# Kernel tuning notes

Hardware: AMD Instinct MI355X
Metric: run time of the kernel (lower is better)

## Reference

```python
import jax, jax.numpy as jnp
import numpy as np

D_STATE = 16
D_CONV = 4


def layernorm(x, g, b, eps=1e-5):
    mu = jnp.mean(x, axis=-1, keepdims=True)
    var = jnp.mean(jnp.square(x - mu), axis=-1, keepdims=True)
    return (x - mu) * jax.lax.rsqrt(var + eps) * g + b


def mamba(x, W_in, conv_w, conv_b, W_x, W_dt, b_dt, A_log, D_param, W_out):
    # x: (B, L, C)
    B, L, C = x.shape
    d_inner, d_conv = conv_w.shape
    d_state = A_log.shape[1]
    dt_rank = W_dt.shape[0]

    xz = x @ W_in                       # (B, L, 2*d_inner)
    xm, z = jnp.split(xz, 2, axis=-1)   # each (B, L, d_inner)

    # depthwise causal conv1d (padding d_conv-1 on the left, truncated to L)
    xp = jnp.pad(xm, ((0, 0), (d_conv - 1, 0), (0, 0)))
    xm = sum(xp[:, k:k + L, :] * conv_w[:, k] for k in range(d_conv)) + conv_b
    xm = jax.nn.silu(xm)

    dbl = xm @ W_x                      # (B, L, dt_rank + 2*d_state)
    dt, Bm, Cm = jnp.split(dbl, [dt_rank, dt_rank + d_state], axis=-1)
    dt = jax.nn.softplus(dt @ W_dt + b_dt)  # (B, L, d_inner)
    A = -jnp.exp(A_log)                     # (d_inner, d_state)

    def step(h, inputs):
        dt_t, B_t, C_t, x_t = inputs        # (B,d_inner),(B,d_state),(B,d_state),(B,d_inner)
        dA = jnp.exp(dt_t[..., None] * A)   # (B, d_inner, d_state)
        h = dA * h + (dt_t * x_t)[..., None] * B_t[:, None, :]
        y = jnp.einsum('bds,bs->bd', h, C_t)
        return h, y

    seq = (dt.transpose(1, 0, 2), Bm.transpose(1, 0, 2),
           Cm.transpose(1, 0, 2), xm.transpose(1, 0, 2))
    h0 = jnp.zeros((B, d_inner, d_state), x.dtype)
    _, ys = jax.lax.scan(step, h0, seq)     # ys: (L, B, d_inner)
    y = ys.transpose(1, 0, 2) + xm * D_param
    y = y * jax.nn.silu(z)
    return y @ W_out                        # (B, L, C)


def setup_inputs() -> dict:
    key = jax.random.key(0)
    B, C, H, W = 8, 256, 32, 32
    d_inner = 2 * C
    dt_rank = (C + 15) // 16  # 16
    hidden = 4 * C
    ks = jax.random.split(key, 12)
    s = lambda k, shape, scale=0.02: jax.random.normal(k, shape, jnp.float32) * scale
    return {
        'x': jax.random.normal(ks[0], (B, C, H, W), jnp.float32),
        'ln1_g': jnp.ones((C,), jnp.float32), 'ln1_b': jnp.zeros((C,), jnp.float32),
        'ln2_g': jnp.ones((C,), jnp.float32), 'ln2_b': jnp.zeros((C,), jnp.float32),
        'W_in': s(ks[1], (C, 2 * d_inner)),
        'conv_w': s(ks[2], (d_inner, D_CONV), 0.1),
        'conv_b': jnp.zeros((d_inner,), jnp.float32),
        'W_x': s(ks[3], (d_inner, dt_rank + 2 * D_STATE)),
        'W_dt': s(ks[4], (dt_rank, d_inner)),
        'b_dt': s(ks[5], (d_inner,), 0.1),
        'A_log': jnp.log(jnp.tile(jnp.arange(1, D_STATE + 1, dtype=jnp.float32), (d_inner, 1))),
        'D_param': jnp.ones((d_inner,), jnp.float32),
        'W_out': s(ks[6], (d_inner, C)),
        'W1': s(ks[7], (C, hidden)), 'b1': jnp.zeros((hidden,), jnp.float32),
        'W2': s(ks[8], (hidden, C)), 'b2': jnp.zeros((C,), jnp.float32),
    }


def reference(x, ln1_g, ln1_b, ln2_g, ln2_b, W_in, conv_w, conv_b, W_x, W_dt,
              b_dt, A_log, D_param, W_out, W1, b1, W2, b2):
    B, C, H, W = x.shape
    x = x.transpose(0, 2, 3, 1)          # (B, H, W, C)
    res = x
    xn = layernorm(x, ln1_g, ln1_b)
    xm = mamba(xn.reshape(B, H * W, C), W_in, conv_w, conv_b, W_x, W_dt,
               b_dt, A_log, D_param, W_out).reshape(B, H, W, C)
    x = xm + res
    res = x
    xn = layernorm(x, ln2_g, ln2_b)
    x = jax.nn.gelu(xn @ W1 + b1, approximate=False) @ W2 + b2 + res
    return x.transpose(0, 3, 1, 2)        # (B, C, H, W)
```

## Files before the change

### kernel.cpp

```cpp
#include <hip/hip_runtime.h>
#include <hip/hip_bf16.h>
#include <math.h>

using u16 = unsigned short;
using u32 = unsigned int;
typedef __attribute__((ext_vector_type(8))) short bf16x8;
typedef __attribute__((ext_vector_type(4))) float f32x4;
typedef __attribute__((ext_vector_type(8))) unsigned short us8;
typedef __attribute__((ext_vector_type(4))) unsigned short us4;

__device__ __forceinline__ float b2f(u16 u) {
  return __uint_as_float(((u32)u) << 16);
}
__device__ __forceinline__ u16 f2b(float f) {
  u32 x = __float_as_uint(f);
  x += 0x7fffu + ((x >> 16) & 1u);
  return (u16)(x >> 16);
}

__global__ void k_detect(const u16* __restrict__ alog, int* __restrict__ flag) {
  if (threadIdx.x == 0 && blockIdx.x == 0)
    flag[0] = (alog[1] != 0) ? 1 : 0;
}

__device__ __forceinline__ u16 cvt_one(const void* src, int i, int f) {
  u16 r;
  if (f == 0) {
    float v = ((const float*)src)[i];
    if (!isfinite(v)) v = 0.f;
    r = f2b(v);
  } else {
    r = ((const u16*)src)[i];
    if (((r >> 7) & 0xFFu) == 0xFFu) r = 0;
  }
  return r;
}

__global__ __launch_bounds__(256) void k_cvtw(const void* __restrict__ s0,
    const void* __restrict__ s1, const void* __restrict__ s2,
    const void* __restrict__ s3, u16* __restrict__ d0, u16* __restrict__ d1,
    u16* __restrict__ d2, u16* __restrict__ d3, const int* __restrict__ flag) {
  int i = blockIdx.x * 256 + threadIdx.x;
  int f = flag[0];
  if (i < 262144) {
    int k = i >> 10, n = i & 1023;
    d0[n * 256 + k] = cvt_one(s0, i, f);
  } else if (i < 524288) {
    int j = i - 262144; int k = j >> 10, n = j & 1023;
    d1[n * 256 + k] = cvt_one(s1, j, f);
  } else if (i < 786432) {
    int j = i - 524288; int k = j >> 8, n = j & 255;
    d2[n * 1024 + k] = cvt_one(s2, j, f);
  } else if (i < 917504) {
    int j = i - 786432; int k = j >> 8, n = j & 255;
    d3[n * 512 + k] = cvt_one(s3, j, f);
  }
}

struct SmallCvt {
  const void* src[13];
  u16* dst[13];
  int end[13];
};
__global__ __launch_bounds__(256) void k_cvt_small(SmallCvt p,
    int total, const int* __restrict__ flag) {
  int i = blockIdx.x * 256 + threadIdx.x;
  if (i >= total) return;
  int f = flag[0];
  int seg = 0, base = 0;
  #pragma unroll
  for (int s = 0; s < 13; ++s) {
    if (i >= p.end[s]) { seg = s + 1; base = p.end[s]; }
  }
  p.dst[seg][i - base] = cvt_one(p.src[seg], i - base, f);
}

__global__ __launch_bounds__(256) void k_tln(const void* __restrict__ src,
    const u16* __restrict__ g, const u16* __restrict__ be,
    u16* __restrict__ xt, u16* __restrict__ xn, const int* __restrict__ flag) {
  __shared__ float t[256][33];
  __shared__ float smu[32], srs[32];
  int bid = blockIdx.x;
  int lt = bid & 31, b = bid >> 5;
  int f = flag[0];
  int lc = threadIdx.x & 31, lr = threadIdx.x >> 5;
  for (int i = 0; i < 32; ++i) {
    int c = i * 8 + lr;
    int l = lt * 32 + lc;
    size_t idx = ((size_t)b * 256 + c) * 1024 + l;
    float v;
    if (f == 0) {
      v = ((const float*)src)[idx];
      if (!isfinite(v)) v = 0.f;
    } else {
      u16 u = ((const u16*)src)[idx];
      if (((u >> 7) & 0xFFu) == 0xFFu) u = 0;
      v = b2f(u);
    }
    t[c][lc] = v;
  }
  __syncthreads();
  int tok = threadIdx.x >> 3, j = threadIdx.x & 7;
  float s = 0.f, q = 0.f;
  for (int k = 0; k < 32; ++k) {
    float v = t[j + 8 * k][tok];
    s += v; q = fmaf(v, v, q);
  }
  s += __shfl_xor(s, 1, 8); q += __shfl_xor(q, 1, 8);
  s += __shfl_xor(s, 2, 8); q += __shfl_xor(q, 2, 8);
  s += __shfl_xor(s, 4, 8); q += __shfl_xor(q, 4, 8);
  if (j == 0) {
    float mu = s * (1.f / 256.f);
    smu[tok] = mu;
    srs[tok] = rsqrtf(q * (1.f / 256.f) - mu * mu + 1e-5f);
  }
  __syncthreads();
  float gv = b2f(g[threadIdx.x]), bv = b2f(be[threadIdx.x]);
  size_t tok0 = (size_t)b * 1024 + lt * 32;
  for (int i = 0; i < 32; ++i) {
    float v = t[threadIdx.x][i];
    size_t o = (tok0 + i) * 256 + threadIdx.x;
    xt[o] = f2b(v);
    xn[o] = f2b((v - smu[i]) * srs[i] * gv + bv);
  }
}

__global__ __launch_bounds__(256) void k_tout(const u16* __restrict__ ytmp,
    void* __restrict__ outp, const int* __restrict__ flag) {
  __shared__ float t[32][33];
  int bid = blockIdx.x;
  int lt = bid & 31, ct = (bid >> 5) & 7, b = bid >> 8;
  int f = flag[0];
  int lc = threadIdx.x & 31, lr = threadIdx.x >> 5;
  #pragma unroll
  for (int r = 0; r < 4; ++r) {
    int l = lt * 32 + lr + r * 8;
    int c = ct * 32 + lc;
    t[lr + r * 8][lc] = b2f(ytmp[((size_t)b * 1024 + l) * 256 + c]);
  }
  __syncthreads();
  #pragma unroll
  for (int r = 0; r < 4; ++r) {
    int c = ct * 32 + lr + r * 8;
    int l = lt * 32 + lc;
    size_t oi = ((size_t)b * 256 + c) * 1024 + l;
    float v = t[lc][lr + r * 8];
    if (f) ((u16*)outp)[oi] = f2b(v);
    else   ((float*)outp)[oi] = v;
  }
}

__global__ __launch_bounds__(256) void k_ln(const u16* __restrict__ xin,
    const u16* __restrict__ g, const u16* __restrict__ be,
    u16* __restrict__ xn) {
  __shared__ float buf[256];
  __shared__ float mv[2];
  int tok = blockIdx.x;
  int c = threadIdx.x;
  float v = b2f(xin[(size_t)tok * 256 + c]);
  buf[c] = v;
  __syncthreads();
  for (int off = 128; off > 0; off >>= 1) {
    if (c < off) buf[c] += buf[c + off];
    __syncthreads();
  }
  if (c == 0) mv[0] = buf[0] * (1.f / 256.f);
  __syncthreads();
  float mu = mv[0];
  float dd = v - mu;
  buf[c] = dd * dd;
  __syncthreads();
  for (int off = 128; off > 0; off >>= 1) {
    if (c < off) buf[c] += buf[c + off];
    __syncthreads();
  }
  if (c == 0) mv[1] = rsqrtf(buf[0] * (1.f / 256.f) + 1e-5f);
  __syncthreads();
  float rs = mv[1];
  xn[(size_t)tok * 256 + c] = f2b(dd * rs * b2f(g[c]) + b2f(be[c]));
}

__global__ __launch_bounds__(256) void k_conv(const u16* __restrict__ xz,
    const u16* __restrict__ cw, const u16* __restrict__ cb,
    u16* __restrict__ xm) {
  int idx = blockIdx.x * 256 + threadIdx.x;
  int d4 = (idx & 127) * 4;
  int tok = idx >> 7;
  int l = tok & 1023;
  float a[4];
  #pragma unroll
  for (int j = 0; j < 4; ++j) a[j] = b2f(cb[d4 + j]);
  #pragma unroll
  for (int k = 0; k < 4; ++k) {
    int ls = l - 3 + k;
    if (ls >= 0) {
      us4 xv = *(const us4*)&xz[(size_t)(tok - 3 + k) * 1024 + d4];
      #pragma unroll
      for (int j = 0; j < 4; ++j)
        a[j] = fmaf(b2f(xv[j]), b2f(cw[(d4 + j) * 4 + k]), a[j]);
    }
  }
  us4 o;
  #pragma unroll
  for (int j = 0; j < 4; ++j) {
    float sig = 1.f / (1.f + __expf(-a[j]));
    o[j] = f2b(a[j] * sig);
  }
  *(us4*)&xm[(size_t)tok * 512 + d4] = o;
}

__global__ __launch_bounds__(256) void k_wc(const u16* __restrict__ Wx,
    const u16* __restrict__ Wdt, u16* __restrict__ wcbc) {
  int idx = blockIdx.x * 256 + threadIdx.x;
  int j = idx >> 9, i = idx & 511;
  u16 r;
  if (j < 512) {
    float s = 0.f;
    #pragma unroll
    for (int k = 0; k < 16; ++k)
      s = fmaf(b2f(Wx[i * 48 + k]), b2f(Wdt[k * 512 + j]), s);
    r = f2b(s);
  } else if (j < 544) {
    r = Wx[i * 48 + 16 + (j - 512)];
  } else {
    r = 0;
  }
  wcbc[idx] = r;
}

__global__ __launch_bounds__(256) void k_scan1(const u16* __restrict__ dt,
    const u16* __restrict__ xm, const u16* __restrict__ bc,
    const u16* __restrict__ A_log, u16* __restrict__ hend,
    float* __restrict__ sdtw) {
  __shared__ float sB[32][16];
  int bi = blockIdx.x;
  int half = bi & 1;
  int bc_ = bi >> 1;
  int b = bc_ >> 5, c = bc_ & 31;
  int d = half * 256 + threadIdx.x;
  size_t tok0 = (size_t)b * 1024 + c * 32;
  for (int i = threadIdx.x; i < 512; i += 256) {
    int t = i >> 4, s = i & 15;
    sB[t][s] = b2f(bc[(tok0 + t) * 32 + s]);
  }
  __syncthreads();
  float As[16], h[16];
  bool fast = true;
  #pragma unroll
  for (int s = 0; s < 16; ++s) {
    As[s] = -__expf(b2f(A_log[d * 16 + s]));
    h[s] = 0.f;
    fast = fast && (fabsf(As[s] + (float)(s + 1)) < 0.02f * (s + 1));
  }
  float sacc = 0.f;
  float dtv = b2f(dt[tok0 * 512 + d]);
  float xv  = b2f(xm[tok0 * 512 + d]);
  if (fast) {
    for (int t = 0; t < 32; ++t) {
      float ndt = 0.f, nx = 0.f;
      if (t < 31) {
        ndt = b2f(dt[(tok0 + t + 1) * 512 + d]);
        nx  = b2f(xm[(tok0 + t + 1) * 512 + d]);
      }
      sacc += dtv;
      float u = dtv * xv;
      float q = __expf(-dtv), p = 1.f;
      #pragma unroll
      for (int s = 0; s < 16; ++s) {
        p *= q;
        h[s] = fmaf(p, h[s], u * sB[t][s]);
      }
      dtv = ndt; xv = nx;
    }
  } else {
    for (int t = 0; t < 32; ++t) {
      float ndt = 0.f, nx = 0.f;
      if (t < 31) {
        ndt = b2f(dt[(tok0 + t + 1) * 512 + d]);
        nx  = b2f(xm[(tok0 + t + 1) * 512 + d]);
      }
      sacc += dtv;
      float u = dtv * xv;
      #pragma unroll
      for (int s = 0; s < 16; ++s)
        h[s] = fmaf(__expf(dtv * As[s]), h[s], u * sB[t][s]);
      dtv = ndt; xv = nx;
    }
  }
  u16* hp = hend + ((size_t)bc_ * 512 + d) * 16;
  #pragma unroll
  for (int s = 0; s < 16; ++s) hp[s] = f2b(h[s]);
  sdtw[(size_t)bc_ * 512 + d] = sacc;
}

__global__ __launch_bounds__(256) void k_scan2(u16* __restrict__ hend,
    const float* __restrict__ sdtw, const u16* __restrict__ A_log) {
  int idx = blockIdx.x * 256 + threadIdx.x;
  int s = idx & 15, d = (idx >> 4) & 511, b = idx >> 13;
  float As_ = -__expf(b2f(A_log[d * 16 + s]));
  if (fabsf(As_ + (float)(s + 1)) < 0.02f * (s + 1)) As_ = -(float)(s + 1);
  float H = 0.f;
  for (int c = 0; c < 32; ++c) {
    size_t off = (size_t)(b * 32 + c) * 512 + d;
    float dec = __expf(As_ * sdtw[off]);
    float he = b2f(hend[off * 16 + s]);
    hend[off * 16 + s] = f2b(H);
    H = fmaf(dec, H, he);
  }
}

__global__ __launch_bounds__(256) void k_scan3(const u16* __restrict__ dt,
    const u16* __restrict__ xm, const u16* __restrict__ bc,
    const u16* __restrict__ xz, const u16* __restrict__ A_log,
    const u16* __restrict__ Dp, const u16* __restrict__ hstart,
    u16* __restrict__ yg) {
  __shared__ float sB[32][16], sC[32][16];
  int bi = blockIdx.x;
  int half = bi & 1;
  int bc_ = bi >> 1;
  int b = bc_ >> 5, c = bc_ & 31;
  int d = half * 256 + threadIdx.x;
  size_t tok0 = (size_t)b * 1024 + c * 32;
  for (int i = threadIdx.x; i < 1024; i += 256) {
    int t = i >> 5, col = i & 31;
    float v = b2f(bc[(tok0 + t) * 32 + col]);
    if (col < 16) sB[t][col] = v;
    else          sC[t][col - 16] = v;
  }
  __syncthreads();
  float As[16], h[16];
  const u16* hp = hstart + ((size_t)bc_ * 512 + d) * 16;
  bool fast = true;
  #pragma unroll
  for (int s = 0; s < 16; ++s) {
    As[s] = -__expf(b2f(A_log[d * 16 + s]));
    h[s] = b2f(hp[s]);
    fast = fast && (fabsf(As[s] + (float)(s + 1)) < 0.02f * (s + 1));
  }
  float Dd = b2f(Dp[d]);
  float dtv = b2f(dt[tok0 * 512 + d]);
  float xv  = b2f(xm[tok0 * 512 + d]);
  float zv  = b2f(xz[tok0 * 1024 + 512 + d]);
  for (int t = 0; t < 32; ++t) {
    float ndt = 0.f, nx = 0.f, nz = 0.f;
    if (t < 31) {
      ndt = b2f(dt[(tok0 + t + 1) * 512 + d]);
      nx  = b2f(xm[(tok0 + t + 1) * 512 + d]);
      nz  = b2f(xz[(tok0 + t + 1) * 1024 + 512 + d]);
    }
    float u = dtv * xv;
    if (fast) {
      float q = __expf(-dtv), p = 1.f;
      #pragma unroll
      for (int s = 0; s < 16; ++s) {
        p *= q;
        h[s] = fmaf(p, h[s], u * sB[t][s]);
      }
    } else {
      #pragma unroll
      for (int s = 0; s < 16; ++s)
        h[s] = fmaf(__expf(dtv * As[s]), h[s], u * sB[t][s]);
    }
    float y0 = 0.f, y1 = 0.f, y2 = 0.f, y3 = 0.f;
    #pragma unroll
    for (int s = 0; s < 16; s += 4) {
      y0 = fmaf(h[s + 0], sC[t][s + 0], y0);
      y1 = fmaf(h[s + 1], sC[t][s + 1], y1);
      y2 = fmaf(h[s + 2], sC[t][s + 2], y2);
      y3 = fmaf(h[s + 3], sC[t][s + 3], y3);
    }
    float y = (y0 + y1) + (y2 + y3);
    float yy = fmaf(xv, Dd, y);
    float sig = 1.f / (1.f + __expf(-zv));
    yg[(tok0 + t) * 512 + d] = f2b(yy * zv * sig);
    dtv = ndt; xv = nx; zv = nz;
  }
}

template<int EPI, int BM, int BN>
__global__ __launch_bounds__(256) void k_mgemm(
    const u16* __restrict__ A, const u16* __restrict__ Bt,
    const u16* __restrict__ bias, const u16* __restrict__ res,
    u16* __restrict__ outp, u16* __restrict__ out2, int M, int N, int K) {
  constexpr int BK = 32;
  constexpr int LDP = BK + 8;
  constexpr int MT = BM / 32, NT = BN / 32;
  constexpr int AL = (BM * BK) / 2048, BL = (BN * BK) / 2048;
  __shared__ u16 As[BM][LDP];
  __shared__ u16 Bs[BN][LDP];
  const int tid = threadIdx.x;
  const int wid = tid >> 6, lane = tid & 63;
  const int wr = wid >> 1, wc2 = wid & 1;
  const int lrow = lane & 15, lk = lane >> 4;
  const int m0 = blockIdx.y * BM, n0 = blockIdx.x * BN;

  f32x4 acc[MT][NT];
  #pragma unroll
  for (int i = 0; i < MT; ++i)
    #pragma unroll
    for (int j = 0; j < NT; ++j)
      acc[i][j] = (f32x4){0.f, 0.f, 0.f, 0.f};

  us8 ra[AL], rb[BL];
  #pragma unroll
  for (int i = 0; i < AL; ++i) {
    int c = tid + i * 256, row = c >> 2, k0 = (c & 3) * 8;
    ra[i] = *(const us8*)(A + (size_t)(m0 + row) * K + k0);
  }
  #pragma unroll
  for (int i = 0; i < BL; ++i) {
    int c = tid + i * 256, row = c >> 2, k0 = (c & 3) * 8;
    rb[i] = *(const us8*)(Bt + (size_t)(n0 + row) * K + k0);
  }

  for (int kb = 0; kb < K; kb += BK) {
    #pragma unroll
    for (int i = 0; i < AL; ++i) {
      int c = tid + i * 256, row = c >> 2, k0 = (c & 3) * 8;
      *(us8*)&As[row][k0] = ra[i];
    }
    #pragma unroll
    for (int i = 0; i < BL; ++i) {
      int c = tid + i * 256, row = c >> 2, k0 = (c & 3) * 8;
      *(us8*)&Bs[row][k0] = rb[i];
    }
    __syncthreads();
    if (kb + BK < K) {
      #pragma unroll
      for (int i = 0; i < AL; ++i) {
        int c = tid + i * 256, row = c >> 2, k0 = (c & 3) * 8;
        ra[i] = *(const us8*)(A + (size_t)(m0 + row) * K + kb + BK + k0);
      }
      #pragma unroll
      for (int i = 0; i < BL; ++i) {
        int c = tid + i * 256, row = c >> 2, k0 = (c & 3) * 8;
        rb[i] = *(const us8*)(Bt + (size_t)(n0 + row) * K + kb + BK + k0);
      }
    }
    bf16x8 af[MT], bf[NT];
    #pragma unroll
    for (int i = 0; i < MT; ++i)
      af[i] = *(const bf16x8*)&As[wr * (BM / 2) + i * 16 + lrow][lk * 8];
    #pragma unroll
    for (int j = 0; j < NT; ++j)
      bf[j] = *(const bf16x8*)&Bs[wc2 * (BN / 2) + j * 16 + lrow][lk * 8];
    #pragma unroll
    for (int i = 0; i < MT; ++i)
      #pragma unroll
      for (int j = 0; j < NT; ++j)
        acc[i][j] = __builtin_amdgcn_mfma_f32_16x16x32_bf16(
            af[i], bf[j], acc[i][j], 0, 0, 0);
    __syncthreads();
  }

  #pragma unroll
  for (int i = 0; i < MT; ++i) {
    #pragma unroll
    for (int j = 0; j < NT; ++j) {
      #pragma unroll
      for (int r = 0; r < 4; ++r) {
        const int m = m0 + wr * (BM / 2) + i * 16 + lk * 4 + r;
        const int n = n0 + wc2 * (BN / 2) + j * 16 + lrow;
        float v = acc[i][j][r];
        if constexpr (EPI == 0) {
          outp[(size_t)m * N + n] = f2b(v);
        } else if constexpr (EPI == 2) {
          float t = v + b2f(res[(size_t)m * N + n]);
          outp[(size_t)m * N + n] = f2b(t);
        } else if constexpr (EPI == 3) {
          float t = v + b2f(bias[n]);
          float gl = 0.5f * t * (1.f + erff(t * 0.70710678118654752f));
          outp[(size_t)m * N + n] = f2b(gl);
        } else if constexpr (EPI == 4) {
          float t = v + b2f(bias[n]) + b2f(res[(size_t)m * N + n]);
          if (!isfinite(t)) t = 0.f;
          outp[(size_t)m * N + n] = f2b(t);
        } else {
          if (n < 512) {
            float t = v + b2f(bias[n]);
            float sp = fmaxf(t, 0.f) + log1pf(__expf(-fabsf(t)));
            outp[(size_t)m * 512 + n] = f2b(sp);
          } else if (n < 544) {
            out2[(size_t)m * 32 + (n - 512)] = f2b(v);
          }
        }
      }
    }
  }
}

extern "C" void kernel_launch(void* const* d_in, const int* in_sizes, int n_in,
                              void* d_out, int out_size, void* d_ws, size_t ws_size,
                              hipStream_t stream) {
  char* ws = (char*)d_ws;
  u16* arena = (u16*)ws;
  u16* x_t  = arena + 0;
  u16* WinT = arena + 2097152;
  u16* W1T  = arena + 2359296;
  u16* W2T  = arena + 2621440;
  u16* WoT  = arena + 2883584;
  u16* WxC  = arena + 3014656;
  u16* WdtC = arena + 3047424;
  const size_t S = 3145728;
  u16* g1C  = arena + S + 0;
  u16* b1nC = arena + S + 256;
  u16* g2C  = arena + S + 512;
  u16* b2nC = arena + S + 768;
  u16* cbC  = arena + S + 1024;
  u16* bdtC = arena + S + 1536;
  u16* DpC  = arena + S + 2048;
  u16* bb2C = arena + S + 2560;
  u16* bb1C = arena + S + 3072;
  u16* cwC  = arena + S + 4096;
  u16* AlC  = arena + S + 6144;
  float* sdtw = (float*)(ws + (7ull << 20));

  u16* xn1 = (u16*)(ws + (8ull  << 20));
  u16* x2  = xn1;
  u16* hend = (u16*)(ws + (8ull << 20));
  u16* xz  = (u16*)(ws + (12ull << 20));
  u16* h1  = xz;
  u16* xm  = (u16*)(ws + (28ull << 20));
  u16* xn2 = xm;
  u16* dtb = (u16*)(ws + (36ull << 20));
  u16* ytmp = dtb;
  u16* yg  = (u16*)(ws + (44ull << 20));
  u16* bcb = (u16*)(ws + (52ull << 20));
  u16* wcbc = (u16*)(ws + (52ull << 20) + (512ull << 10));
  int* flag = (int*)(ws + (54ull << 20));

  k_detect<<<1, 64, 0, stream>>>((const u16*)d_in[11], flag);
  k_cvtw<<<3584, 256, 0, stream>>>(d_in[5], d_in[14], d_in[16], d_in[13],
                                   WinT, W1T, W2T, WoT, flag);
  {
    SmallCvt p;
    const int ids[13] = {1, 2, 3, 4, 6, 7, 8, 9, 10, 11, 12, 15, 17};
    u16* dsts[13] = {g1C, b1nC, g2C, b2nC, cwC, cbC, WxC, WdtC, bdtC, AlC, DpC, bb1C, bb2C};
    int acc = 0;
    for (int i = 0; i < 13; ++i) {
      p.src[i] = d_in[ids[i]];
      p.dst[i] = dsts[i];
      acc += in_sizes[ids[i]];
      p.end[i] = acc;
    }
    k_cvt_small<<<(acc + 255) / 256, 256, 0, stream>>>(p, acc, flag);
  }
  k_wc<<<1152, 256, 0, stream>>>(WxC, WdtC, wcbc);

  k_tln<<<256, 256, 0, stream>>>(d_in[0], g1C, b1nC, x_t, xn1, flag);
  k_mgemm<0, 128, 128><<<dim3(8, 64), 256, 0, stream>>>(
      xn1, WinT, nullptr, nullptr, xz, nullptr, 8192, 1024, 256);
  k_conv<<<4096, 256, 0, stream>>>(xz, cwC, cbC, xm);
  k_mgemm<5, 128, 64><<<dim3(9, 64), 256, 0, stream>>>(
      xm, wcbc, bdtC, nullptr, dtb, bcb, 8192, 576, 512);
  k_scan1<<<512, 256, 0, stream>>>(dtb, xm, bcb, AlC, hend, sdtw);
  k_scan2<<<256, 256, 0, stream>>>(hend, sdtw, AlC);
  k_scan3<<<512, 256, 0, stream>>>(dtb, xm, bcb, xz, AlC, DpC, hend, yg);
  k_mgemm<2, 64, 64><<<dim3(4, 128), 256, 0, stream>>>(
      yg, WoT, nullptr, x_t, x2, nullptr, 8192, 256, 512);
  k_ln<<<8192, 256, 0, stream>>>(x2, g2C, b2nC, xn2);
  k_mgemm<3, 128, 128><<<dim3(8, 64), 256, 0, stream>>>(
      xn2, W1T, bb1C, nullptr, h1, nullptr, 8192, 1024, 256);
  k_mgemm<4, 64, 64><<<dim3(4, 128), 256, 0, stream>>>(
      h1, W2T, bb2C, x2, ytmp, nullptr, 8192, 256, 1024);
  k_tout<<<2048, 256, 0, stream>>>(ytmp, d_out, flag);
}
```

Baseline: 289.7 us.

## Fuse setup conversions, fold output transpose into GEMM epilogue, warp-level layernorm

Merges the weight-conversion, small-parameter-conversion and W_x·W_dt combine kernels into one setup kernel, which removes two launches. The final GEMM epilogue now transposes through shared memory and writes the (B,C,H,W) output directly, so the separate transpose kernel and its bf16 round trip are gone. The second layernorm now uses one wave per token with shuffle reductions instead of a shared-memory tree with many barriers. The first transpose-layernorm kernel moves to 16-token tiles to launch more blocks. The costs are extra shared memory in the fused epilogue and recomputed conversions of W_x and W_dt inside the combine step.

```diff
diff --git a/kernel.cpp b/kernel.cpp
--- a/kernel.cpp
+++ b/kernel.cpp
@@ -36,57 +36,75 @@
   return r;
 }
 
-__global__ __launch_bounds__(256) void k_cvtw(const void* __restrict__ s0,
-    const void* __restrict__ s1, const void* __restrict__ s2,
-    const void* __restrict__ s3, u16* __restrict__ d0, u16* __restrict__ d1,
-    u16* __restrict__ d2, u16* __restrict__ d3, const int* __restrict__ flag) {
+struct SetupP {
+  const void* ws0; const void* ws1; const void* ws2; const void* ws3;
+  u16* wd0; u16* wd1; u16* wd2; u16* wd3;
+  const void* ssrc[11];
+  u16* sdst[11];
+  int send[11];
+  const void* wxr;
+  const void* wdtr;
+  u16* wcbc;
+  int smallEnd;
+  int total;
+};
+__global__ __launch_bounds__(256) void k_setup(SetupP p, const int* __restrict__ flag) {
   int i = blockIdx.x * 256 + threadIdx.x;
+  if (i >= p.total) return;
   int f = flag[0];
   if (i < 262144) {
     int k = i >> 10, n = i & 1023;
-    d0[n * 256 + k] = cvt_one(s0, i, f);
+    p.wd0[n * 256 + k] = cvt_one(p.ws0, i, f);
   } else if (i < 524288) {
     int j = i - 262144; int k = j >> 10, n = j & 1023;
-    d1[n * 256 + k] = cvt_one(s1, j, f);
+    p.wd1[n * 256 + k] = cvt_one(p.ws1, j, f);
   } else if (i < 786432) {
     int j = i - 524288; int k = j >> 8, n = j & 255;
-    d2[n * 1024 + k] = cvt_one(s2, j, f);
+    p.wd2[n * 1024 + k] = cvt_one(p.ws2, j, f);
   } else if (i < 917504) {
     int j = i - 786432; int k = j >> 8, n = j & 255;
-    d3[n * 512 + k] = cvt_one(s3, j, f);
-  }
-}
-
-struct SmallCvt {
-  const void* src[13];
-  u16* dst[13];
-  int end[13];
-};
-__global__ __launch_bounds__(256) void k_cvt_small(SmallCvt p,
-    int total, const int* __restrict__ flag) {
-  int i = blockIdx.x * 256 + threadIdx.x;
-  if (i >= total) return;
-  int f = flag[0];
-  int seg = 0, base = 0;
-  #pragma unroll
-  for (int s = 0; s < 13; ++s) {
-    if (i >= p.end[s]) { seg = s + 1; base = p.end[s]; }
-  }
-  p.dst[seg][i - base] = cvt_one(p.src[seg], i - base, f);
+    p.wd3[n * 512 + k] = cvt_one(p.ws3, j, f);
+  } else if (i < p.smallEnd) {
+    int j = i - 917504;
+    int seg = 0, base = 0;
+    #pragma unroll
+    for (int s = 0; s < 11; ++s) {
+      if (j >= p.send[s]) { seg = s + 1; base = p.send[s]; }
+    }
+    p.sdst[seg][j - base] = cvt_one(p.ssrc[seg], j - base, f);
+  } else {
+    int idx = i - p.smallEnd;
+    int j = idx >> 9, ii = idx & 511;
+    u16 r;
+    if (j < 512) {
+      float s = 0.f;
+      #pragma unroll
+      for (int k = 0; k < 16; ++k)
+        s = fmaf(b2f(cvt_one(p.wxr, ii * 48 + k, f)),
+                 b2f(cvt_one(p.wdtr, k * 512 + j, f)), s);
+      r = f2b(s);
+    } else if (j < 544) {
+      r = cvt_one(p.wxr, ii * 48 + 16 + (j - 512), f);
+    } else {
+      r = 0;
+    }
+    p.wcbc[idx] = r;
+  }
 }
 
 __global__ __launch_bounds__(256) void k_tln(const void* __restrict__ src,
     const u16* __restrict__ g, const u16* __restrict__ be,
     u16* __restrict__ xt, u16* __restrict__ xn, const int* __restrict__ flag) {
-  __shared__ float t[256][33];
-  __shared__ float smu[32], srs[32];
+  __shared__ float t[256][17];
+  __shared__ float smu[16], srs[16];
   int bid = blockIdx.x;
-  int lt = bid & 31, b = bid >> 5;
+  int lt = bid & 63, b = bid >> 6;
   int f = flag[0];
-  int lc = threadIdx.x & 31, lr = threadIdx.x >> 5;
-  for (int i = 0; i < 32; ++i) {
-    int c = i * 8 + lr;
-    int l = lt * 32 + lc;
+  int lc = threadIdx.x & 15;
+  int lr = threadIdx.x >> 4;
+  for (int i = 0; i < 16; ++i) {
+    int c = i * 16 + lr;
+    int l = lt * 16 + lc;
     size_t idx = ((size_t)b * 256 + c) * 1024 + l;
     float v;
     if (f == 0) {
@@ -100,24 +118,25 @@
     t[c][lc] = v;
   }
   __syncthreads();
-  int tok = threadIdx.x >> 3, j = threadIdx.x & 7;
+  int token = threadIdx.x >> 4, j = threadIdx.x & 15;
   float s = 0.f, q = 0.f;
-  for (int k = 0; k < 32; ++k) {
-    float v = t[j + 8 * k][tok];
+  for (int k = 0; k < 16; ++k) {
+    float v = t[k * 16 + j][token];
     s += v; q = fmaf(v, v, q);
   }
-  s += __shfl_xor(s, 1, 8); q += __shfl_xor(q, 1, 8);
-  s += __shfl_xor(s, 2, 8); q += __shfl_xor(q, 2, 8);
-  s += __shfl_xor(s, 4, 8); q += __shfl_xor(q, 4, 8);
+  s += __shfl_xor(s, 1, 16); q += __shfl_xor(q, 1, 16);
+  s += __shfl_xor(s, 2, 16); q += __shfl_xor(q, 2, 16);
+  s += __shfl_xor(s, 4, 16); q += __shfl_xor(q, 4, 16);
+  s += __shfl_xor(s, 8, 16); q += __shfl_xor(q, 8, 16);
   if (j == 0) {
     float mu = s * (1.f / 256.f);
-    smu[tok] = mu;
-    srs[tok] = rsqrtf(q * (1.f / 256.f) - mu * mu + 1e-5f);
+    smu[token] = mu;
+    srs[token] = rsqrtf(q * (1.f / 256.f) - mu * mu + 1e-5f);
   }
   __syncthreads();
   float gv = b2f(g[threadIdx.x]), bv = b2f(be[threadIdx.x]);
-  size_t tok0 = (size_t)b * 1024 + lt * 32;
-  for (int i = 0; i < 32; ++i) {
+  size_t tok0 = (size_t)b * 1024 + lt * 16;
+  for (int i = 0; i < 16; ++i) {
     float v = t[threadIdx.x][i];
     size_t o = (tok0 + i) * 256 + threadIdx.x;
     xt[o] = f2b(v);
@@ -125,59 +144,33 @@
   }
 }
 
-__global__ __launch_bounds__(256) void k_tout(const u16* __restrict__ ytmp,
-    void* __restrict__ outp, const int* __restrict__ flag) {
-  __shared__ float t[32][33];
-  int bid = blockIdx.x;
-  int lt = bid & 31, ct = (bid >> 5) & 7, b = bid >> 8;
-  int f = flag[0];
-  int lc = threadIdx.x & 31, lr = threadIdx.x >> 5;
-  #pragma unroll
-  for (int r = 0; r < 4; ++r) {
-    int l = lt * 32 + lr + r * 8;
-    int c = ct * 32 + lc;
-    t[lr + r * 8][lc] = b2f(ytmp[((size_t)b * 1024 + l) * 256 + c]);
-  }
-  __syncthreads();
-  #pragma unroll
-  for (int r = 0; r < 4; ++r) {
-    int c = ct * 32 + lr + r * 8;
-    int l = lt * 32 + lc;
-    size_t oi = ((size_t)b * 256 + c) * 1024 + l;
-    float v = t[lc][lr + r * 8];
-    if (f) ((u16*)outp)[oi] = f2b(v);
-    else   ((float*)outp)[oi] = v;
-  }
-}
-
 __global__ __launch_bounds__(256) void k_ln(const u16* __restrict__ xin,
     const u16* __restrict__ g, const u16* __restrict__ be,
     u16* __restrict__ xn) {
-  __shared__ float buf[256];
-  __shared__ float mv[2];
-  int tok = blockIdx.x;
-  int c = threadIdx.x;
-  float v = b2f(xin[(size_t)tok * 256 + c]);
-  buf[c] = v;
-  __syncthreads();
-  for (int off = 128; off > 0; off >>= 1) {
-    if (c < off) buf[c] += buf[c + off];
-    __syncthreads();
-  }
-  if (c == 0) mv[0] = buf[0] * (1.f / 256.f);
-  __syncthreads();
-  float mu = mv[0];
-  float dd = v - mu;
-  buf[c] = dd * dd;
-  __syncthreads();
-  for (int off = 128; off > 0; off >>= 1) {
-    if (c < off) buf[c] += buf[c + off];
-    __syncthreads();
-  }
-  if (c == 0) mv[1] = rsqrtf(buf[0] * (1.f / 256.f) + 1e-5f);
-  __syncthreads();
-  float rs = mv[1];
-  xn[(size_t)tok * 256 + c] = f2b(dd * rs * b2f(g[c]) + b2f(be[c]));
+  int tok = blockIdx.x * 4 + (threadIdx.x >> 6);
+  int lane = threadIdx.x & 63;
+  us4 xv = *(const us4*)&xin[(size_t)tok * 256 + lane * 4];
+  float v[4];
+  float s = 0.f, q = 0.f;
+  #pragma unroll
+  for (int j2 = 0; j2 < 4; ++j2) {
+    v[j2] = b2f(xv[j2]);
+    s += v[j2]; q = fmaf(v[j2], v[j2], q);
+  }
+  #pragma unroll
+  for (int o = 1; o < 64; o <<= 1) {
+    s += __shfl_xor(s, o, 64);
+    q += __shfl_xor(q, o, 64);
+  }
+  float mu = s * (1.f / 256.f);
+  float rs = rsqrtf(q * (1.f / 256.f) - mu * mu + 1e-5f);
+  us4 o4;
+  #pragma unroll
+  for (int j2 = 0; j2 < 4; ++j2) {
+    float t = (v[j2] - mu) * rs * b2f(g[lane * 4 + j2]) + b2f(be[lane * 4 + j2]);
+    o4[j2] = f2b(t);
+  }
+  *(us4*)&xn[(size_t)tok * 256 + lane * 4] = o4;
 }
 
 __global__ __launch_bounds__(256) void k_conv(const u16* __restrict__ xz,
@@ -207,25 +200,6 @@
     o[j] = f2b(a[j] * sig);
   }
   *(us4*)&xm[(size_t)tok * 512 + d4] = o;
-}
-
-__global__ __launch_bounds__(256) void k_wc(const u16* __restrict__ Wx,
-    const u16* __restrict__ Wdt, u16* __restrict__ wcbc) {
-  int idx = blockIdx.x * 256 + threadIdx.x;
-  int j = idx >> 9, i = idx & 511;
-  u16 r;
-  if (j < 512) {
-    float s = 0.f;
-    #pragma unroll
-    for (int k = 0; k < 16; ++k)
-      s = fmaf(b2f(Wx[i * 48 + k]), b2f(Wdt[k * 512 + j]), s);
-    r = f2b(s);
-  } else if (j < 544) {
-    r = Wx[i * 48 + 16 + (j - 512)];
-  } else {
-    r = 0;
-  }
-  wcbc[idx] = r;
 }
 
 __global__ __launch_bounds__(256) void k_scan1(const u16* __restrict__ dt,
@@ -381,7 +355,9 @@
 __global__ __launch_bounds__(256) void k_mgemm(
     const u16* __restrict__ A, const u16* __restrict__ Bt,
     const u16* __restrict__ bias, const u16* __restrict__ res,
-    u16* __restrict__ outp, u16* __restrict__ out2, int M, int N, int K) {
+    u16* __restrict__ outp, u16* __restrict__ out2,
+    void* __restrict__ outv, const int* __restrict__ flag,
+    int M, int N, int K) {
   constexpr int BK = 32;
   constexpr int LDP = BK + 8;
   constexpr int MT = BM / 32, NT = BN / 32;
@@ -451,6 +427,45 @@
         acc[i][j] = __builtin_amdgcn_mfma_f32_16x16x32_bf16(
             af[i], bf[j], acc[i][j], 0, 0, 0);
     __syncthreads();
+  }
+
+  if constexpr (EPI == 6) {
+    __shared__ float tbuf[64][65];
+    #pragma unroll
+    for (int i = 0; i < MT; ++i)
+      #pragma unroll
+      for (int j = 0; j < NT; ++j)
+        #pragma unroll
+        for (int r = 0; r < 4; ++r) {
+          const int ml = wr * (BM / 2) + i * 16 + lk * 4 + r;
+          const int nl = wc2 * (BN / 2) + j * 16 + lrow;
+          float t = acc[i][j][r] + b2f(bias[n0 + nl])
+                  + b2f(res[(size_t)(m0 + ml) * N + n0 + nl]);
+          if (!isfinite(t)) t = 0.f;
+          tbuf[nl][ml] = t;
+        }
+    __syncthreads();
+    int cl = tid >> 2, tg = tid & 3;
+    int c = n0 + cl;
+    int bb = m0 >> 10;
+    int l0 = (m0 & 1023) + tg * 16;
+    size_t obase = ((size_t)bb * 256 + c) * 1024 + l0;
+    int f = flag[0];
+    if (f) {
+      us8 o0, o1;
+      #pragma unroll
+      for (int k = 0; k < 8; ++k) {
+        o0[k] = f2b(tbuf[cl][tg * 16 + k]);
+        o1[k] = f2b(tbuf[cl][tg * 16 + 8 + k]);
+      }
+      *(us8*)((u16*)outv + obase) = o0;
+      *(us8*)((u16*)outv + obase + 8) = o1;
+    } else {
+      float* op = (float*)outv + obase;
+      #pragma unroll
+      for (int k = 0; k < 16; ++k) op[k] = tbuf[cl][tg * 16 + k];
+    }
+    return;
   }
 
   #pragma unroll
@@ -471,11 +486,7 @@
           float t = v + b2f(bias[n]);
           float gl = 0.5f * t * (1.f + erff(t * 0.70710678118654752f));
           outp[(size_t)m * N + n] = f2b(gl);
-        } else if constexpr (EPI == 4) {
-          float t = v + b2f(bias[n]) + b2f(res[(size_t)m * N + n]);
-          if (!isfinite(t)) t = 0.f;
-          outp[(size_t)m * N + n] = f2b(t);
-        } else {
+        } else if constexpr (EPI == 5) {
           if (n < 512) {
             float t = v + b2f(bias[n]);
             float sp = fmaxf(t, 0.f) + log1pf(__expf(-fabsf(t)));
@@ -499,8 +510,6 @@
   u16* W1T  = arena + 2359296;
   u16* W2T  = arena + 2621440;
   u16* WoT  = arena + 2883584;
-  u16* WxC  = arena + 3014656;
-  u16* WdtC = arena + 3047424;
   const size_t S = 3145728;
   u16* g1C  = arena + S + 0;
   u16* b1nC = arena + S + 256;
@@ -523,45 +532,49 @@
   u16* xm  = (u16*)(ws + (28ull << 20));
   u16* xn2 = xm;
   u16* dtb = (u16*)(ws + (36ull << 20));
-  u16* ytmp = dtb;
   u16* yg  = (u16*)(ws + (44ull << 20));
   u16* bcb = (u16*)(ws + (52ull << 20));
   u16* wcbc = (u16*)(ws + (52ull << 20) + (512ull << 10));
   int* flag = (int*)(ws + (54ull << 20));
 
   k_detect<<<1, 64, 0, stream>>>((const u16*)d_in[11], flag);
-  k_cvtw<<<3584, 256, 0, stream>>>(d_in[5], d_in[14], d_in[16], d_in[13],
-                                   WinT, W1T, W2T, WoT, flag);
   {
-    SmallCvt p;
-    const int ids[13] = {1, 2, 3, 4, 6, 7, 8, 9, 10, 11, 12, 15, 17};
-    u16* dsts[13] = {g1C, b1nC, g2C, b2nC, cwC, cbC, WxC, WdtC, bdtC, AlC, DpC, bb1C, bb2C};
+    SetupP p;
+    p.ws0 = d_in[5];  p.wd0 = WinT;
+    p.ws1 = d_in[14]; p.wd1 = W1T;
+    p.ws2 = d_in[16]; p.wd2 = W2T;
+    p.ws3 = d_in[13]; p.wd3 = WoT;
+    const int ids[11] = {1, 2, 3, 4, 6, 7, 10, 11, 12, 15, 17};
+    u16* dsts[11] = {g1C, b1nC, g2C, b2nC, cwC, cbC, bdtC, AlC, DpC, bb1C, bb2C};
     int acc = 0;
-    for (int i = 0; i < 13; ++i) {
-      p.src[i] = d_in[ids[i]];
-      p.dst[i] = dsts[i];
+    for (int i = 0; i < 11; ++i) {
+      p.ssrc[i] = d_in[ids[i]];
+      p.sdst[i] = dsts[i];
       acc += in_sizes[ids[i]];
-      p.end[i] = acc;
-    }
-    k_cvt_small<<<(acc + 255) / 256, 256, 0, stream>>>(p, acc, flag);
-  }
-  k_wc<<<1152, 256, 0, stream>>>(WxC, WdtC, wcbc);
-
-  k_tln<<<256, 256, 0, stream>>>(d_in[0], g1C, b1nC, x_t, xn1, flag);
+      p.send[i] = acc;
+    }
+    p.wxr = d_in[8];
+    p.wdtr = d_in[9];
+    p.wcbc = wcbc;
+    p.smallEnd = 917504 + acc;
+    p.total = p.smallEnd + 294912;
+    k_setup<<<(p.total + 255) / 256, 256, 0, stream>>>(p, flag);
+  }
+
+  k_tln<<<512, 256, 0, stream>>>(d_in[0], g1C, b1nC, x_t, xn1, flag);
   k_mgemm<0, 128, 128><<<dim3(8, 64), 256, 0, stream>>>(
-      xn1, WinT, nullptr, nullptr, xz, nullptr, 8192, 1024, 256);
+      xn1, WinT, nullptr, nullptr, xz, nullptr, nullptr, flag, 8192, 1024, 256);
   k_conv<<<4096, 256, 0, stream>>>(xz, cwC, cbC, xm);
   k_mgemm<5, 128, 64><<<dim3(9, 64), 256, 0, stream>>>(
-      xm, wcbc, bdtC, nullptr, dtb, bcb, 8192, 576, 512);
+      xm, wcbc, bdtC, nullptr, dtb, bcb, nullptr, flag, 8192, 576, 512);
   k_scan1<<<512, 256, 0, stream>>>(dtb, xm, bcb, AlC, hend, sdtw);
   k_scan2<<<256, 256, 0, stream>>>(hend, sdtw, AlC);
   k_scan3<<<512, 256, 0, stream>>>(dtb, xm, bcb, xz, AlC, DpC, hend, yg);
   k_mgemm<2, 64, 64><<<dim3(4, 128), 256, 0, stream>>>(
-      yg, WoT, nullptr, x_t, x2, nullptr, 8192, 256, 512);
-  k_ln<<<8192, 256, 0, stream>>>(x2, g2C, b2nC, xn2);
+      yg, WoT, nullptr, x_t, x2, nullptr, nullptr, flag, 8192, 256, 512);
+  k_ln<<<2048, 256, 0, stream>>>(x2, g2C, b2nC, xn2);
   k_mgemm<3, 128, 128><<<dim3(8, 64), 256, 0, stream>>>(
-      xn2, W1T, bb1C, nullptr, h1, nullptr, 8192, 1024, 256);
-  k_mgemm<4, 64, 64><<<dim3(4, 128), 256, 0, stream>>>(
-      h1, W2T, bb2C, x2, ytmp, nullptr, 8192, 256, 1024);
-  k_tout<<<2048, 256, 0, stream>>>(ytmp, d_out, flag);
-}
+      xn2, W1T, bb1C, nullptr, h1, nullptr, nullptr, flag, 8192, 1024, 256);
+  k_mgemm<6, 64, 64><<<dim3(4, 128), 256, 0, stream>>>(
+      h1, W2T, bb2C, x2, nullptr, nullptr, d_out, flag, 8192, 256, 1024);
+}
```

New measurement: 282.6 us. -2.4%, faster.
